# Optimization experiments

Measured on AMD Instinct MI355X. Metric: run time of the kernel, lower is better.

Reference implementation:

```python
import jax, jax.numpy as jnp
import numpy as np

D_MODEL = 1024
NUM_HEADS = 16
HEAD_DIM = D_MODEL // NUM_HEADS
MASK_FUTURE = False
NEG_INF = -1.0e9


def setup_inputs() -> dict:
    key = jax.random.key(0)
    ks = jax.random.split(key, 8)
    B, L = 2, 2048
    q = jax.random.normal(ks[0], (B, L, D_MODEL), dtype=jnp.float32)
    k = jax.random.normal(ks[1], (B, L, D_MODEL), dtype=jnp.float32)
    v = jax.random.normal(ks[2], (B, L, D_MODEL), dtype=jnp.float32)
    attention_mask = jnp.ones((B, L), dtype=jnp.int32)
    s = 1.0 / np.sqrt(D_MODEL)
    Wq = jax.random.normal(ks[3], (D_MODEL, D_MODEL), dtype=jnp.float32) * s
    Wk = jax.random.normal(ks[4], (D_MODEL, D_MODEL), dtype=jnp.float32) * s
    Wv = jax.random.normal(ks[5], (D_MODEL, D_MODEL), dtype=jnp.float32) * s
    Wo = jax.random.normal(ks[6], (D_MODEL, D_MODEL), dtype=jnp.float32) * s
    return {"q": q, "k": k, "v": v, "attention_mask": attention_mask,
            "Wq": Wq, "Wk": Wk, "Wv": Wv, "Wo": Wo}


def _split_heads(x):
    B, L, _ = x.shape
    return x.reshape(B, L, NUM_HEADS, HEAD_DIM).transpose(0, 2, 1, 3)  # [B,H,L,Hd]


def reference(q, k, v, attention_mask, Wq, Wk, Wv, Wo):
    B, Lq, _ = q.shape
    Lk = k.shape[1]
    Q = _split_heads(q @ Wq.T)
    K = _split_heads(k @ Wk.T)
    V = _split_heads(v @ Wv.T)
    scale = HEAD_DIM ** 0.5  # per-head D in original Attention
    scores = jnp.einsum('bhqd,bhkd->bhqk', Q, K) / scale
    mask = (attention_mask == 0)[:, None, None, :]  # [B,1,1,Lk]
    scores = jnp.where(mask, NEG_INF, scores)
    if MASK_FUTURE:
        fut = jnp.triu(jnp.ones((Lq, Lk), dtype=bool), k=1)
        scores = jnp.where(fut[None, None], NEG_INF, scores)
    attn = jax.nn.softmax(scores, axis=-1)
    out = jnp.einsum('bhqk,bhkd->bhqd', attn, V)
    out = out.transpose(0, 2, 1, 3).reshape(B, Lq, D_MODEL)
    return out @ Wo.T
```

## Files before the change

### kernel.cpp

```cpp
#include <hip/hip_runtime.h>


#define D_MODEL 1024
#define NH 16
#define HD 64
#define BATCH 2
#define SEQ 2048
#define MROWS (BATCH*SEQ)

typedef unsigned short u16;
typedef __bf16 bf16x8 __attribute__((ext_vector_type(8)));
typedef float f32x4 __attribute__((ext_vector_type(4)));
typedef float f32x16 __attribute__((ext_vector_type(16)));

__device__ __forceinline__ u16 f2bf(float f){
    __bf16 h = (__bf16)f;
    return __builtin_bit_cast(u16, h);
}
__device__ __forceinline__ float fast_exp2(float x){ return __builtin_amdgcn_exp2f(x); }

__device__ __forceinline__ void stage16(const void* g, void* l){
#if __has_builtin(__builtin_amdgcn_global_load_lds)
    __builtin_amdgcn_global_load_lds(
        (__attribute__((address_space(1))) void*)(unsigned long long)(g),
        (__attribute__((address_space(3))) void*)(unsigned int)(unsigned long long)(l),
        16, 0, 0);
#else
    *(uint4*)l = *(const uint4*)g;
#endif
}

__device__ __forceinline__ int detect_f32_block(const u16* q, int tid){
    __shared__ int flag;
    if (tid < 64){
        unsigned e = (q[2*tid]>>7)&0xFFu;
        bool hit = (e>=115u)&&(e<=132u);
        unsigned long long m = __ballot(hit);
        if (tid==0) flag = (__popcll(m) < 32) ? 1 : 0;
    }
    __syncthreads();
    return flag;
}

__global__ __launch_bounds__(256)
void convert_all(const u16* __restrict__ q, const u16* __restrict__ k,
                 const u16* __restrict__ v, const u16* __restrict__ Wq,
                 const u16* __restrict__ Wk, const u16* __restrict__ Wv,
                 const u16* __restrict__ Wo, u16* __restrict__ dst)
{
    int isf32 = detect_f32_block(q, threadIdx.x);
    int bid = blockIdx.x;
    const u16* src; int lb;
    if      (bid < 4096)  { src=q;  lb=bid; }
    else if (bid < 8192)  { src=k;  lb=bid-4096; }
    else if (bid < 12288) { src=v;  lb=bid-8192; }
    else if (bid < 13312) { src=Wq; lb=bid-12288; }
    else if (bid < 14336) { src=Wk; lb=bid-13312; }
    else if (bid < 15360) { src=Wv; lb=bid-14336; }
    else                  { src=Wo; lb=bid-15360; }
    size_t so = (size_t)lb*1024 + threadIdx.x*4;
    size_t dofs = (size_t)bid*1024 + threadIdx.x*4;
    if (isf32){
        float4 x = *(const float4*)((const float*)src + so);
        ushort4 o; o.x=f2bf(x.x); o.y=f2bf(x.y); o.z=f2bf(x.z); o.w=f2bf(x.w);
        *(ushort4*)(dst+dofs) = o;
    } else {
        *(ushort4*)(dst+dofs) = *(const ushort4*)(src+so);
    }
}

__global__ __launch_bounds__(256)
void gemm_qkv(const u16* __restrict__ qb, const u16* __restrict__ kb,
              const u16* __restrict__ vb, const u16* __restrict__ Wqb,
              const u16* __restrict__ Wkb, const u16* __restrict__ Wvb,
              u16* __restrict__ Qh, u16* __restrict__ Kh, u16* __restrict__ Vt)
{
    const int K = 1024;
    __shared__ __align__(16) u16 lA[128*32];
    __shared__ __align__(16) u16 lB[128*32];
    const int z = blockIdx.z;
    const u16* A  = (z==0)? qb  : (z==1)? kb  : vb;
    const u16* Bt = (z==0)? Wqb : (z==1)? Wkb : Wvb;

    const int tid  = threadIdx.x;
    const int wid  = tid>>6, lane = tid&63;
    const int quad = lane>>4, l16 = lane&15;
    const int wm = (wid>>1)*64, wn = (wid&1)*64;
    const int row0 = blockIdx.y*128, col0 = blockIdx.x*128;

    f32x4 acc[4][4];
    #pragma unroll
    for (int i=0;i<4;i++)
        #pragma unroll
        for (int j=0;j<4;j++) acc[i][j] = (f32x4){0.f,0.f,0.f,0.f};

    for (int k0=0; k0<K; k0+=32){
        #pragma unroll
        for (int s=0;s<2;s++){
            int c = tid + s*256;
            int r = c>>2, cc = (c&3)*8;
            stage16(&A [(size_t)(row0+r)*K + k0 + cc], &lA[c*8]);
            stage16(&Bt[(size_t)(col0+r)*K + k0 + cc], &lB[c*8]);
        }
        __syncthreads();
        bf16x8 af[4], bfr[4];
        #pragma unroll
        for (int mi=0;mi<4;mi++) af[mi]  = *(const bf16x8*)&lA[(wm+mi*16+l16)*32 + quad*8];
        #pragma unroll
        for (int ni=0;ni<4;ni++) bfr[ni] = *(const bf16x8*)&lB[(wn+ni*16+l16)*32 + quad*8];
        #pragma unroll
        for (int mi=0;mi<4;mi++)
            #pragma unroll
            for (int ni=0;ni<4;ni++)
                acc[mi][ni] = __builtin_amdgcn_mfma_f32_16x16x32_bf16(af[mi], bfr[ni], acc[mi][ni], 0,0,0);
        __syncthreads();
    }

    const float qsc = (z==0) ? 0.18033688011112042f : 1.0f;
    u16* Csh = (z==0)? Qh : Kh;
    #pragma unroll
    for (int mi=0;mi<4;mi++){
        #pragma unroll
        for (int ni=0;ni<4;ni++){
            int col = col0 + wn + ni*16 + l16;
            #pragma unroll
            for (int r=0;r<4;r++){
                int row = row0 + wm + mi*16 + quad*4 + r;
                u16 o = f2bf(acc[mi][ni][r]*qsc);
                int b = row>>11, i = row&2047, h = col>>6, d = col&63;
                if (z<2) Csh[((((size_t)(b*NH+h))*SEQ + i)<<6) + d] = o;
                else     Vt[((size_t)((b*NH+h)*HD + d))*SEQ + i] = o;
            }
        }
    }
}

__global__ __launch_bounds__(256)
void gemm_out(const u16* __restrict__ A, const u16* __restrict__ Bt,
              void* __restrict__ Cv, const u16* __restrict__ qref)
{
    const int K = 1024, N = 1024;
    int outf32 = detect_f32_block(qref, threadIdx.x);
    __shared__ __align__(16) u16 lA[64*32];
    __shared__ __align__(16) u16 lB[128*32];
    const int tid  = threadIdx.x;
    const int wid  = tid>>6, lane = tid&63;
    const int quad = lane>>4, l16 = lane&15;
    const int wm = (wid>>1)*32, wn = (wid&1)*64;
    const int row0 = blockIdx.y*64, col0 = blockIdx.x*128;

    f32x4 acc[2][4];
    #pragma unroll
    for (int i=0;i<2;i++)
        #pragma unroll
        for (int j=0;j<4;j++) acc[i][j] = (f32x4){0.f,0.f,0.f,0.f};

    for (int k0=0; k0<K; k0+=32){
        {
            int r = tid>>2, cc = (tid&3)*8;
            stage16(&A[(size_t)(row0+r)*K + k0 + cc], &lA[tid*8]);
        }
        #pragma unroll
        for (int s=0;s<2;s++){
            int c = tid + s*256;
            int r = c>>2, cc = (c&3)*8;
            stage16(&Bt[(size_t)(col0+r)*K + k0 + cc], &lB[c*8]);
        }
        __syncthreads();
        bf16x8 af[2], bfr[4];
        #pragma unroll
        for (int mi=0;mi<2;mi++) af[mi]  = *(const bf16x8*)&lA[(wm+mi*16+l16)*32 + quad*8];
        #pragma unroll
        for (int ni=0;ni<4;ni++) bfr[ni] = *(const bf16x8*)&lB[(wn+ni*16+l16)*32 + quad*8];
        #pragma unroll
        for (int mi=0;mi<2;mi++)
            #pragma unroll
            for (int ni=0;ni<4;ni++)
                acc[mi][ni] = __builtin_amdgcn_mfma_f32_16x16x32_bf16(af[mi], bfr[ni], acc[mi][ni], 0,0,0);
        __syncthreads();
    }

    #pragma unroll
    for (int mi=0;mi<2;mi++){
        #pragma unroll
        for (int ni=0;ni<4;ni++){
            int col = col0 + wn + ni*16 + l16;
            #pragma unroll
            for (int r=0;r<4;r++){
                int row = row0 + wm + mi*16 + quad*4 + r;
                float f = acc[mi][ni][r];
                if (outf32) ((float*)Cv)[(size_t)row*N + col] = f;
                else        ((u16*)Cv)[(size_t)row*N + col] = f2bf(f);
            }
        }
    }
}

#define KVT 4096
#define SW(row, c8) ((row)*64 + ((((c8) ^ ((row)&7)))*8))

__device__ __forceinline__ bf16x8 ldv_nat(const u16* lvc, int row, int chunk2, int hi){
    uint2 lo = *(const uint2*)&lvc[SW(row, chunk2)   + 4*hi];
    uint2 hj = *(const uint2*)&lvc[SW(row, chunk2+1) + 4*hi];
    union { uint4 u; bf16x8 v; } r;
    r.u.x = lo.x; r.u.y = lo.y; r.u.z = hj.x; r.u.w = hj.y;
    return r.v;
}

__global__ __launch_bounds__(256)
void attn3(const u16* __restrict__ Qh, const u16* __restrict__ Kh,
           const u16* __restrict__ Vt, const int* __restrict__ mask,
           u16* __restrict__ ctx)
{
    __shared__ __align__(16) u16 lk[2*KVT];
    __shared__ __align__(16) u16 lv[2*KVT];
    __shared__ unsigned mb[64];

    const int id = blockIdx.x;
    const int bh = (id&7)*4 + (id>>7);
    const int qb = (id>>3)&15;
    const int b = bh>>4, h = bh&15;
    const int i0 = qb*128;
    const int tid = threadIdx.x;
    const int wv = tid>>6, lane = tid&63;
    const int l31 = lane&31, hi = lane>>5;

    const u16* Kp  = Kh + (size_t)bh*SEQ*HD;
    const u16* Vtp = Vt + (size_t)bh*HD*SEQ;
    const int* mp  = mask + b*SEQ;

    if (tid < 64){
        unsigned w = 0;
        #pragma unroll 8
        for (int i=0;i<32;i++) w |= (mp[tid*32+i] ? 1u:0u) << i;
        mb[tid] = w;
    }
    #pragma unroll
    for (int s=0;s<2;s++){
        int c = tid + s*256;
        int r = c>>3, c8 = c&7;
        *(uint4*)&lk[SW(r,c8)] = *(const uint4*)&Kp[(size_t)r*HD + c8*8];
        *(uint4*)&lv[SW(r,c8)] = *(const uint4*)&Vtp[(size_t)r*SEQ + c8*8];
    }

    const u16* Qrow = Qh + ((size_t)bh*SEQ + i0 + wv*32 + l31)*HD;
    bf16x8 aq[4];
    #pragma unroll
    for (int kk=0;kk<4;kk++) aq[kk] = *(const bf16x8*)&Qrow[kk*16 + hi*8];

    bf16x8 bones;
    #pragma unroll
    for (int j=0;j<8;j++) ((u16*)&bones)[j] = 0x3F80;

    f32x16 Oacc[2], Lacc;
    #pragma unroll
    for (int r=0;r<16;r++){ Oacc[0][r]=0.f; Oacc[1][r]=0.f; Lacc[r]=0.f; }

    for (int t=0; t<32; t++){
        const int j0 = t*64;
        const u16* lkc = lk + (t&1)*KVT;
        const u16* lvc = lv + (t&1)*KVT;
        u16* lkn = lk + ((t&1)^1)*KVT;
        u16* lvn = lv + ((t&1)^1)*KVT;

        __syncthreads();

        uint4 gk[2], gv[2];
        if (t < 31){
            #pragma unroll
            for (int s=0;s<2;s++){
                int c = tid + s*256;
                int r = c>>3, c8 = c&7;
                gk[s] = *(const uint4*)&Kp[(size_t)(j0+64+r)*HD + c8*8];
                gv[s] = *(const uint4*)&Vtp[(size_t)r*SEQ + j0+64 + c8*8];
            }
        }

        __builtin_amdgcn_s_setprio(1);
        #pragma unroll
        for (int jt=0; jt<2; ++jt){
            f32x16 sfr;
            #pragma unroll
            for (int r=0;r<16;r++) sfr[r]=0.f;
            #pragma unroll
            for (int kk=0;kk<4;kk++){
                bf16x8 ak = *(const bf16x8*)&lkc[SW(jt*32+l31, 2*kk+hi)];
                sfr = __builtin_amdgcn_mfma_f32_32x32x16_bf16(ak, aq[kk], sfr, 0,0,0);
            }

            unsigned mw = mb[2*t+jt];
            if ((unsigned)__builtin_amdgcn_readfirstlane((int)mw) != 0xFFFFFFFFu){
                unsigned ms = mw >> (hi*4);
                #pragma unroll
                for (int r=0;r<16;r++){
                    int kb = (r&3)+8*(r>>2);
                    if (!((ms>>kb)&1u)) sfr[r] = -1.0e9f;
                }
            }

            unsigned cc[8];
            #pragma unroll
            for (int d=0; d<8; ++d){
                float p0 = fast_exp2(sfr[2*d]);
                float p1 = fast_exp2(sfr[2*d+1]);
                cc[d] = (unsigned)f2bf(p0) | ((unsigned)f2bf(p1)<<16);
            }
            bf16x8 pa0, pa1;
            ((unsigned*)&pa0)[0]=cc[0]; ((unsigned*)&pa0)[1]=cc[1];
            ((unsigned*)&pa0)[2]=cc[2]; ((unsigned*)&pa0)[3]=cc[3];
            ((unsigned*)&pa1)[0]=cc[4]; ((unsigned*)&pa1)[1]=cc[5];
            ((unsigned*)&pa1)[2]=cc[6]; ((unsigned*)&pa1)[3]=cc[7];

            Lacc = __builtin_amdgcn_mfma_f32_32x32x16_bf16(pa0, bones, Lacc, 0,0,0);
            Lacc = __builtin_amdgcn_mfma_f32_32x32x16_bf16(pa1, bones, Lacc, 0,0,0);

            #pragma unroll
            for (int dn=0; dn<2; ++dn){
                int vr = dn*32 + l31;
                bf16x8 bv0 = ldv_nat(lvc, vr, jt*4,   hi);
                bf16x8 bv1 = ldv_nat(lvc, vr, jt*4+2, hi);
                Oacc[dn] = __builtin_amdgcn_mfma_f32_32x32x16_bf16(pa0, bv0, Oacc[dn], 0,0,0);
                Oacc[dn] = __builtin_amdgcn_mfma_f32_32x32x16_bf16(pa1, bv1, Oacc[dn], 0,0,0);
            }
        }
        __builtin_amdgcn_s_setprio(0);

        if (t < 31){
            #pragma unroll
            for (int s=0;s<2;s++){
                int c = tid + s*256;
                int r = c>>3, c8 = c&7;
                *(uint4*)&lkn[SW(r,c8)] = gk[s];
                *(uint4*)&lvn[SW(r,c8)] = gv[s];
            }
        }
    }

    float rc[16];
    #pragma unroll
    for (int r=0;r<16;r++) rc[r] = 1.0f / Lacc[r];
    #pragma unroll
    for (int dn=0; dn<2; ++dn){
        int col = h*HD + dn*32 + l31;
        #pragma unroll
        for (int r=0;r<16;r++){
            int row = i0 + wv*32 + (r&3) + 8*(r>>2) + 4*hi;
            ctx[((size_t)(b*SEQ+row))*D_MODEL + col] = f2bf(Oacc[dn][r] * rc[r]);
        }
    }
}

extern "C" void kernel_launch(void* const* d_in, const int* in_sizes, int n_in,
                              void* d_out, int out_size, void* d_ws, size_t ws_size,
                              hipStream_t stream)
{
    (void)in_sizes; (void)n_in; (void)out_size; (void)ws_size;
    const u16* q    = (const u16*)d_in[0];
    const u16* k    = (const u16*)d_in[1];
    const u16* v    = (const u16*)d_in[2];
    const int* mask = (const int*)d_in[3];
    const u16* Wq   = (const u16*)d_in[4];
    const u16* Wk   = (const u16*)d_in[5];
    const u16* Wv   = (const u16*)d_in[6];
    const u16* Wo   = (const u16*)d_in[7];

    const size_t TEN = (size_t)MROWS * D_MODEL;
    const size_t WEL = (size_t)D_MODEL * D_MODEL;
    u16* qb  = (u16*)d_ws;
    u16* kb  = qb + TEN;
    u16* vb  = kb + TEN;
    u16* Wqb = vb + TEN;
    u16* Wkb = Wqb + WEL;
    u16* Wvb = Wkb + WEL;
    u16* Wob = Wvb + WEL;
    u16* Qh  = Wob + WEL;
    u16* Kh  = Qh + TEN;
    u16* Vtr = Kh + TEN;
    u16* ctx = Vtr + TEN;

    dim3 bb(256);
    convert_all<<<dim3(16384), bb, 0, stream>>>(q,k,v,Wq,Wk,Wv,Wo, qb);
    gemm_qkv<<<dim3(8,32,3), bb, 0, stream>>>(qb,kb,vb, Wqb,Wkb,Wvb, Qh,Kh,Vtr);
    attn3<<<dim3(512), bb, 0, stream>>>(Qh, Kh, Vtr, mask, ctx);
    gemm_out<<<dim3(8,64), bb, 0, stream>>>(ctx, Wob, d_out, q);
}
```

Baseline: 261.5 us.

## Split attention KV range across two half-blocks and merge partial sums in LDS

```diff
diff --git a/kernel.cpp b/kernel.cpp
--- a/kernel.cpp
+++ b/kernel.cpp
@@ -197,23 +197,16 @@
 }
 
 #define KVT 4096
+#define VROW 68
+#define VVT (64*VROW)
 #define SW(row, c8) ((row)*64 + ((((c8) ^ ((row)&7)))*8))
 
-__device__ __forceinline__ bf16x8 ldv_nat(const u16* lvc, int row, int chunk2, int hi){
-    uint2 lo = *(const uint2*)&lvc[SW(row, chunk2)   + 4*hi];
-    uint2 hj = *(const uint2*)&lvc[SW(row, chunk2+1) + 4*hi];
-    union { uint4 u; bf16x8 v; } r;
-    r.u.x = lo.x; r.u.y = lo.y; r.u.z = hj.x; r.u.w = hj.y;
-    return r.v;
-}
-
-__global__ __launch_bounds__(256)
+__global__ __launch_bounds__(512, 4)
 void attn3(const u16* __restrict__ Qh, const u16* __restrict__ Kh,
            const u16* __restrict__ Vt, const int* __restrict__ mask,
            u16* __restrict__ ctx)
 {
-    __shared__ __align__(16) u16 lk[2*KVT];
-    __shared__ __align__(16) u16 lv[2*KVT];
+    __shared__ __align__(16) u16 smem[4*KVT + 4*VVT];
     __shared__ unsigned mb[64];
 
     const int id = blockIdx.x;
@@ -224,9 +217,15 @@
     const int tid = threadIdx.x;
     const int wv = tid>>6, lane = tid&63;
     const int l31 = lane&31, hi = lane>>5;
-
-    const u16* Kp  = Kh + (size_t)bh*SEQ*HD;
-    const u16* Vtp = Vt + (size_t)bh*HD*SEQ;
+    const int hf = tid>>8;
+    const int lt = tid&255;
+    const int wq = wv&3;
+
+    u16* lkh = smem + (hf*2)*KVT;
+    u16* lvh = smem + 4*KVT + (hf*2)*VVT;
+
+    const u16* Kp  = Kh + (size_t)bh*SEQ*HD + (size_t)hf*1024*HD;
+    const u16* Vtp = Vt + (size_t)bh*HD*SEQ + hf*1024;
     const int* mp  = mask + b*SEQ;
 
     if (tid < 64){
@@ -237,13 +236,17 @@
     }
     #pragma unroll
     for (int s=0;s<2;s++){
-        int c = tid + s*256;
+        int c = lt + s*256;
         int r = c>>3, c8 = c&7;
-        *(uint4*)&lk[SW(r,c8)] = *(const uint4*)&Kp[(size_t)r*HD + c8*8];
-        *(uint4*)&lv[SW(r,c8)] = *(const uint4*)&Vtp[(size_t)r*SEQ + c8*8];
-    }
-
-    const u16* Qrow = Qh + ((size_t)bh*SEQ + i0 + wv*32 + l31)*HD;
+        *(uint4*)&lkh[SW(r,c8)] = *(const uint4*)&Kp[(size_t)r*HD + c8*8];
+        uint4 x = *(const uint4*)&Vtp[(size_t)r*SEQ + c8*8];
+        uint2 xl; xl.x = x.x; xl.y = x.y;
+        uint2 xh; xh.x = x.z; xh.y = x.w;
+        *(uint2*)&lvh[r*VROW + c8*8]     = xl;
+        *(uint2*)&lvh[r*VROW + c8*8 + 4] = xh;
+    }
+
+    const u16* Qrow = Qh + ((size_t)bh*SEQ + i0 + wq*32 + l31)*HD;
     bf16x8 aq[4];
     #pragma unroll
     for (int kk=0;kk<4;kk++) aq[kk] = *(const bf16x8*)&Qrow[kk*16 + hi*8];
@@ -256,23 +259,22 @@
     #pragma unroll
     for (int r=0;r<16;r++){ Oacc[0][r]=0.f; Oacc[1][r]=0.f; Lacc[r]=0.f; }
 
-    for (int t=0; t<32; t++){
-        const int j0 = t*64;
-        const u16* lkc = lk + (t&1)*KVT;
-        const u16* lvc = lv + (t&1)*KVT;
-        u16* lkn = lk + ((t&1)^1)*KVT;
-        u16* lvn = lv + ((t&1)^1)*KVT;
+    for (int t=0; t<16; t++){
+        u16* lkc = lkh + (t&1)*KVT;
+        u16* lvc = lvh + (t&1)*VVT;
+        u16* lkn = lkh + ((t&1)^1)*KVT;
+        u16* lvn = lvh + ((t&1)^1)*VVT;
 
         __syncthreads();
 
         uint4 gk[2], gv[2];
-        if (t < 31){
+        if (t < 15){
             #pragma unroll
             for (int s=0;s<2;s++){
-                int c = tid + s*256;
+                int c = lt + s*256;
                 int r = c>>3, c8 = c&7;
-                gk[s] = *(const uint4*)&Kp[(size_t)(j0+64+r)*HD + c8*8];
-                gv[s] = *(const uint4*)&Vtp[(size_t)r*SEQ + j0+64 + c8*8];
+                gk[s] = *(const uint4*)&Kp[(size_t)(t*64+64+r)*HD + c8*8];
+                gv[s] = *(const uint4*)&Vtp[(size_t)r*SEQ + t*64+64 + c8*8];
             }
         }
 
@@ -288,7 +290,7 @@
                 sfr = __builtin_amdgcn_mfma_f32_32x32x16_bf16(ak, aq[kk], sfr, 0,0,0);
             }
 
-            unsigned mw = mb[2*t+jt];
+            unsigned mw = mb[(hf*16+t)*2 + jt];
             if ((unsigned)__builtin_amdgcn_readfirstlane((int)mw) != 0xFFFFFFFFu){
                 unsigned ms = mw >> (hi*4);
                 #pragma unroll
@@ -316,36 +318,63 @@
 
             #pragma unroll
             for (int dn=0; dn<2; ++dn){
-                int vr = dn*32 + l31;
-                bf16x8 bv0 = ldv_nat(lvc, vr, jt*4,   hi);
-                bf16x8 bv1 = ldv_nat(lvc, vr, jt*4+2, hi);
-                Oacc[dn] = __builtin_amdgcn_mfma_f32_32x32x16_bf16(pa0, bv0, Oacc[dn], 0,0,0);
-                Oacc[dn] = __builtin_amdgcn_mfma_f32_32x32x16_bf16(pa1, bv1, Oacc[dn], 0,0,0);
+                int vrb = (dn*32 + l31)*VROW + jt*32 + 4*hi;
+                uint2 a0 = *(const uint2*)&lvc[vrb];
+                uint2 a1 = *(const uint2*)&lvc[vrb + 8];
+                uint2 b0 = *(const uint2*)&lvc[vrb + 16];
+                uint2 b1 = *(const uint2*)&lvc[vrb + 24];
+                union { uint4 u; bf16x8 v; } bv0, bv1;
+                bv0.u.x=a0.x; bv0.u.y=a0.y; bv0.u.z=a1.x; bv0.u.w=a1.y;
+                bv1.u.x=b0.x; bv1.u.y=b0.y; bv1.u.z=b1.x; bv1.u.w=b1.y;
+                Oacc[dn] = __builtin_amdgcn_mfma_f32_32x32x16_bf16(pa0, bv0.v, Oacc[dn], 0,0,0);
+                Oacc[dn] = __builtin_amdgcn_mfma_f32_32x32x16_bf16(pa1, bv1.v, Oacc[dn], 0,0,0);
             }
         }
         __builtin_amdgcn_s_setprio(0);
 
-        if (t < 31){
+        if (t < 15){
             #pragma unroll
             for (int s=0;s<2;s++){
-                int c = tid + s*256;
+                int c = lt + s*256;
                 int r = c>>3, c8 = c&7;
                 *(uint4*)&lkn[SW(r,c8)] = gk[s];
-                *(uint4*)&lvn[SW(r,c8)] = gv[s];
-            }
-        }
-    }
-
-    float rc[16];
-    #pragma unroll
-    for (int r=0;r<16;r++) rc[r] = 1.0f / Lacc[r];
-    #pragma unroll
-    for (int dn=0; dn<2; ++dn){
-        int col = h*HD + dn*32 + l31;
-        #pragma unroll
-        for (int r=0;r<16;r++){
-            int row = i0 + wv*32 + (r&3) + 8*(r>>2) + 4*hi;
-            ctx[((size_t)(b*SEQ+row))*D_MODEL + col] = f2bf(Oacc[dn][r] * rc[r]);
+                uint2 xl; xl.x = gv[s].x; xl.y = gv[s].y;
+                uint2 xh; xh.x = gv[s].z; xh.y = gv[s].w;
+                *(uint2*)&lvn[r*VROW + c8*8]     = xl;
+                *(uint2*)&lvn[r*VROW + c8*8 + 4] = xh;
+            }
+        }
+    }
+
+    __syncthreads();
+    float* mrg = (float*)smem;
+    if (hf == 1){
+        float* p = mrg + (size_t)(wq*64 + lane)*49;
+        #pragma unroll
+        for (int dn=0; dn<2; ++dn)
+            #pragma unroll
+            for (int r=0;r<16;r++) p[dn*16+r] = Oacc[dn][r];
+        #pragma unroll
+        for (int r=0;r<16;r++) p[32+r] = Lacc[r];
+    }
+    __syncthreads();
+    if (hf == 0){
+        const float* p = mrg + (size_t)(wq*64 + lane)*49;
+        #pragma unroll
+        for (int dn=0; dn<2; ++dn)
+            #pragma unroll
+            for (int r=0;r<16;r++) Oacc[dn][r] += p[dn*16+r];
+        float rc[16];
+        #pragma unroll
+        for (int r=0;r<16;r++) rc[r] = 1.0f / (Lacc[r] + p[32+r]);
+        #pragma unroll
+        for (int dn=0; dn<2; ++dn){
+            int col = h*HD + dn*32 + l31;
+            #pragma unroll
+            for (int r=0;r<16;r++){
+                int row = i0 + wq*32 + (r&3) + 8*(r>>2) + 4*hi;
+                ctx[((size_t)(b*SEQ+row))*D_MODEL + col] = f2bf(Oacc[dn][r] * rc[r]);
+            }
         }
     }
 }
@@ -381,6 +410,6 @@
     dim3 bb(256);
     convert_all<<<dim3(16384), bb, 0, stream>>>(q,k,v,Wq,Wk,Wv,Wo, qb);
     gemm_qkv<<<dim3(8,32,3), bb, 0, stream>>>(qb,kb,vb, Wqb,Wkb,Wvb, Qh,Kh,Vtr);
-    attn3<<<dim3(512), bb, 0, stream>>>(Qh, Kh, Vtr, mask, ctx);
+    attn3<<<dim3(512), dim3(512), 0, stream>>>(Qh, Kh, Vtr, mask, ctx);
     gemm_out<<<dim3(8,64), bb, 0, stream>>>(ctx, Wob, d_out, q);
 }
```

Measured after the change: 227.2 us. 1.15x faster.
